# Kernel tuning notes

Hardware: AMD Instinct MI355X
Metric: run time of the kernel (lower is better)

Reference implementation:

```python
import jax, jax.numpy as jnp
import numpy as np

B, Lq, Lk = 2, 4096, 1024
Q_DIM, KV_DIM = 2048, 2048
H, HD = 16, 128          # n_heads, head_dim (nope part)
KVC, QC, R = 512, 768, 64  # kv_comp_dim, q_comp_dim, retr_dim (RoPE part)
LOOKBACK = 8
NEG = -1e30


def setup_inputs() -> dict:
    key = jax.random.key(0)
    ks = jax.random.split(key, 11)
    def w(k, shape, fan_in):
        return jax.random.normal(k, shape, jnp.float32) / np.sqrt(fan_in).astype(np.float32)
    return {
        'q': jax.random.normal(ks[0], (B, Lq, Q_DIM), jnp.float32),
        'kv': jax.random.normal(ks[1], (B, Lk, KV_DIM), jnp.float32),
        'seg_id': jnp.sort(jax.random.randint(ks[2], (B, Lq), 0, Lk), axis=-1),
        'W_kvc': w(ks[3], (KV_DIM, KVC), KV_DIM),   # kv_comp linear (no bias)
        'W_dq':  w(ks[4], (Q_DIM, QC), Q_DIM),      # query down-projection
        'W_uq':  w(ks[5], (QC, H * HD), QC),        # query up-proj (nope)
        'W_qr':  w(ks[6], (QC, H * R), QC),         # query rope proj
        'W_uk':  w(ks[7], (KVC, H * HD), KVC),      # key up-proj (nope)
        'W_kr':  w(ks[8], (KVC, R), KVC),           # shared key rope proj
        'W_uv':  w(ks[9], (KVC, H * HD), KVC),      # value up-proj
        'W_o':   w(ks[10], (H * HD, Q_DIM), H * HD),# output projection
    }


def _rope(x, L):
    # x: [..., L, R] with R even; positions 0..L-1 on the -2 axis.
    half = x.shape[-1] // 2
    inv_freq = 1.0 / (10000.0 ** (jnp.arange(half, dtype=jnp.float32) / half))
    ang = jnp.arange(L, dtype=jnp.float32)[:, None] * inv_freq  # [L, half]
    cos, sin = jnp.cos(ang), jnp.sin(ang)
    x1, x2 = x[..., :half], x[..., half:]
    return jnp.concatenate([x1 * cos - x2 * sin, x1 * sin + x2 * cos], axis=-1)


def reference(q, kv, seg_id, W_kvc, W_dq, W_uq, W_qr, W_uk, W_kr, W_uv, W_o):
    b, lq, _ = q.shape
    lk = kv.shape[1]
    kv_c = kv @ W_kvc                                   # [B,Lk,KVC]
    q_c = q @ W_dq                                      # [B,Lq,QC]
    q_nope = (q_c @ W_uq).reshape(b, lq, H, HD).transpose(0, 2, 1, 3)  # [B,H,Lq,HD]
    q_rope = (q_c @ W_qr).reshape(b, lq, H, R).transpose(0, 2, 1, 3)   # [B,H,Lq,R]
    k_nope = (kv_c @ W_uk).reshape(b, lk, H, HD)        # [B,Lk,H,HD]
    v = (kv_c @ W_uv).reshape(b, lk, H, HD)             # [B,Lk,H,HD]
    k_rope = kv_c @ W_kr                                # [B,Lk,R] shared across heads
    q_rope = _rope(q_rope, lq)
    k_rope = _rope(k_rope, lk)
    scale = 1.0 / np.sqrt(HD + R).astype(np.float32)
    scores = (jnp.einsum('bhqd,bkhd->bhqk', q_nope, k_nope)
              + jnp.einsum('bhqr,bkr->bhqk', q_rope, k_rope)) * scale
    # segment lookback block mask: allow q_seg - lookback <= k <= q_seg
    k_ids = jnp.arange(lk)[None, None, :]               # [1,1,Lk]
    qs = seg_id[:, :, None]                             # [B,Lq,1]
    good = (k_ids <= qs) & (k_ids >= qs - LOOKBACK)     # [B,Lq,Lk]
    scores = jnp.where(good[:, None, :, :], scores, NEG)
    attn = jax.nn.softmax(scores, axis=-1)              # [B,H,Lq,Lk]
    out = jnp.einsum('bhqk,bkhd->bqhd', attn, v).reshape(b, lq, H * HD)
    return out @ W_o                                    # [B,Lq,Q_DIM]
```

## Files before the change

### kernel.cpp

```cpp
#include <hip/hip_runtime.h>
#include <math.h>

typedef __bf16 bf16_t;
typedef __bf16 bf16x8 __attribute__((ext_vector_type(8)));
typedef float f32x4 __attribute__((ext_vector_type(4)));

#define B_    2
#define LQ    4096
#define LK    1024
#define QDIM  2048
#define KVDIM 2048
#define H_    16
#define HD_   128
#define KVC_  512
#define QC_   768
#define R_    64

#define QCOMB 3072
#define KCOMB 4352

#define NL_ROPE (-9.210340371976184f / 32.0f)

typedef __attribute__((address_space(1))) void gvoid_t;
typedef __attribute__((address_space(3))) void lvoid_t;

static __device__ __forceinline__ void gld_lds16(const void* g, void* l) {
  __builtin_amdgcn_global_load_lds((gvoid_t*)(void*)g, (lvoid_t*)l, 16, 0, 0);
}

static __device__ __forceinline__ float fexp(float x) {
  return __builtin_amdgcn_exp2f(x * 1.4426950408889634f);
}
static __device__ __forceinline__ void fsincos(float ang, float* s, float* c) {
  float rev = ang * 0.15915494309189535f;
  rev -= floorf(rev);
  *s = __builtin_amdgcn_sinf(rev);
  *c = __builtin_amdgcn_cosf(rev);
}

struct TransAll {
  const float* src[8];
  bf16_t* dst[8];
  int K[8], N[8], gx[8];
  int off[9];
};

#define NCVT 4096
__global__ __launch_bounds__(256) void prep_all(
    const float* __restrict__ qa, bf16_t* __restrict__ oq, long nq,
    const float* __restrict__ kva, bf16_t* __restrict__ okv, long nkv,
    TransAll d) {
  __shared__ float t[32][33];
  const int bid = blockIdx.x;
  if (bid < NCVT) {
    const long stride = (long)NCVT * 256 * 8;
    for (long i = ((long)bid * 256 + threadIdx.x) * 8; i < nq; i += stride) {
      float4 x = *(const float4*)(qa + i);
      float4 y = *(const float4*)(qa + i + 4);
      bf16x8 v;
      v[0] = (bf16_t)x.x; v[1] = (bf16_t)x.y; v[2] = (bf16_t)x.z; v[3] = (bf16_t)x.w;
      v[4] = (bf16_t)y.x; v[5] = (bf16_t)y.y; v[6] = (bf16_t)y.z; v[7] = (bf16_t)y.w;
      *(bf16x8*)(oq + i) = v;
    }
    for (long i = ((long)bid * 256 + threadIdx.x) * 8; i < nkv; i += stride) {
      float4 x = *(const float4*)(kva + i);
      float4 y = *(const float4*)(kva + i + 4);
      bf16x8 v;
      v[0] = (bf16_t)x.x; v[1] = (bf16_t)x.y; v[2] = (bf16_t)x.z; v[3] = (bf16_t)x.w;
      v[4] = (bf16_t)y.x; v[5] = (bf16_t)y.y; v[6] = (bf16_t)y.z; v[7] = (bf16_t)y.w;
      *(bf16x8*)(okv + i) = v;
    }
    return;
  }
  const int tb = bid - NCVT;
  int i = 0;
#pragma unroll
  for (int j = 1; j < 8; ++j) if (tb >= d.off[j]) i = j;
  const float* __restrict__ src = d.src[i];
  bf16_t* __restrict__ dst = d.dst[i];
  const int K = d.K[i], N = d.N[i];
  const int local = tb - d.off[i];
  const int gx = d.gx[i];
  const int bx = (local % gx) * 32, by = (local / gx) * 32;
  const int x = threadIdx.x & 31, y = threadIdx.x >> 5;
#pragma unroll
  for (int j = 0; j < 32; j += 8)
    t[y + j][x] = src[(size_t)(by + y + j) * N + bx + x];
  __syncthreads();
#pragma unroll
  for (int j = 0; j < 32; j += 8)
    dst[(size_t)(bx + y + j) * K + by + x] = (bf16_t)t[x][y + j];
}

template <int TN, typename CT>
__device__ __forceinline__ void big2_body(
    const bf16_t* __restrict__ A, const bf16_t* __restrict__ Bt, CT* __restrict__ C,
    int N, int K, int row0, int col0, bf16_t* lA, bf16_t* lB) {
  constexpr int NF = TN / 64;
  constexpr int LW = 4 + TN / 64;
  const int tid = threadIdx.x;
  const int w = tid >> 6, lane = tid & 63;
  const int wm = w >> 2, wn = w & 3;
  const int lr = lane >> 3;
  const int kswz = ((lane & 7) ^ lr) * 8;
  const int nt = K >> 6;
  const int fr = lane & 15, fq = lane >> 4;

  auto STAGE = [&](int t, int buf) {
    const int k0 = t << 6;
#pragma unroll
    for (int j = 0; j < 4; ++j) {
      const int s = j * 8 + w;
      gld_lds16(A + (size_t)(row0 + s * 8 + lr) * K + k0 + kswz, &lA[buf * 256 * 64 + s * 512]);
    }
#pragma unroll
    for (int j = 0; j < TN / 64; ++j) {
      const int s = j * 8 + w;
      gld_lds16(Bt + (size_t)(col0 + s * 8 + lr) * K + k0 + kswz, &lB[buf * TN * 64 + s * 512]);
    }
  };

  bf16x8 aA[8], bA[NF], aB[8], bB[NF];
  f32x4 acc[8][NF];
#pragma unroll
  for (int i = 0; i < 8; ++i)
#pragma unroll
    for (int j = 0; j < NF; ++j) acc[i][j] = f32x4{0.f, 0.f, 0.f, 0.f};

  auto READ = [&](int buf, int kk, bf16x8* a, bf16x8* b) {
    const int swzk = (kk * 32 + fq * 8) ^ ((fr & 7) << 3);
#pragma unroll
    for (int mf = 0; mf < 8; ++mf)
      a[mf] = *(const bf16x8*)&lA[buf * 256 * 64 + (wm * 128 + mf * 16 + fr) * 64 + swzk];
#pragma unroll
    for (int nf = 0; nf < NF; ++nf)
      b[nf] = *(const bf16x8*)&lB[buf * TN * 64 + (wn * (TN / 4) + nf * 16 + fr) * 64 + swzk];
  };
  auto MF = [&](bf16x8* a, bf16x8* b) {
    __builtin_amdgcn_s_setprio(1);
#pragma unroll
    for (int mf = 0; mf < 8; ++mf)
#pragma unroll
      for (int nf = 0; nf < NF; ++nf)
        acc[mf][nf] = __builtin_amdgcn_mfma_f32_16x16x32_bf16(a[mf], b[nf], acc[mf][nf], 0, 0, 0);
    __builtin_amdgcn_s_setprio(0);
  };

  STAGE(0, 0);
  STAGE(1, 1);
  if constexpr (LW == 8) { asm volatile("s_waitcnt vmcnt(8)" ::: "memory"); }
  else                   { asm volatile("s_waitcnt vmcnt(6)" ::: "memory"); }
  __builtin_amdgcn_sched_barrier(0);
  __builtin_amdgcn_s_barrier();
  READ(0, 0, aA, bA);

  for (int t = 0; t < nt; ++t) {
    const int buf = t & 1;
    READ(buf, 1, aB, bB);
    __builtin_amdgcn_sched_barrier(0);
    MF(aA, bA);
    asm volatile("s_waitcnt lgkmcnt(0)" ::: "memory");
    __builtin_amdgcn_sched_barrier(0);
    __builtin_amdgcn_s_barrier();
    if (t + 2 < nt) {
      STAGE(t + 2, buf);
      if constexpr (LW == 8) { asm volatile("s_waitcnt vmcnt(8)" ::: "memory"); }
      else                   { asm volatile("s_waitcnt vmcnt(6)" ::: "memory"); }
    } else {
      asm volatile("s_waitcnt vmcnt(0)" ::: "memory");
    }
    __builtin_amdgcn_sched_barrier(0);
    __builtin_amdgcn_s_barrier();
    if (t + 1 < nt) READ(buf ^ 1, 0, aA, bA);
    __builtin_amdgcn_sched_barrier(0);
    MF(aB, bB);
  }

#pragma unroll
  for (int mf = 0; mf < 8; ++mf)
#pragma unroll
    for (int nf = 0; nf < NF; ++nf) {
      const int col = col0 + wn * (TN / 4) + nf * 16 + fr;
#pragma unroll
      for (int r = 0; r < 4; ++r) {
        const int row = row0 + wm * 128 + mf * 16 + fq * 4 + r;
        C[(size_t)row * N + col] = (CT)acc[mf][nf][r];
      }
    }
}

__global__ __launch_bounds__(512, 2) void gemm_dual(
    const bf16_t* __restrict__ A0, const bf16_t* __restrict__ B0, bf16_t* __restrict__ C0,
    int N0, int K0,
    const bf16_t* __restrict__ A1, const bf16_t* __restrict__ B1, bf16_t* __restrict__ C1,
    int N1, int K1, int split) {
  __shared__ __align__(16) bf16_t lA[2 * 256 * 64];
  __shared__ __align__(16) bf16_t lB[2 * 128 * 64];
  const int nwg = gridDim.x;
  const int orig = blockIdx.x;
  const int wg = (orig & 7) * (nwg >> 3) + (orig >> 3);
  if (wg < split) {
    const int gx = N0 / 128;
    big2_body<128, bf16_t>(A0, B0, C0, N0, K0, (wg / gx) * 256, (wg % gx) * 128, lA, lB);
  } else {
    const int l = wg - split;
    const int gx = N1 / 128;
    big2_body<128, bf16_t>(A1, B1, C1, N1, K1, (l / gx) * 256, (l % gx) * 128, lA, lB);
  }
}

#define SWZK_(ks) (((ks) * 32 + fq * 8) ^ ((fr & 7) << 3))
#define RD_A(buf, q) { _Pragma("unroll") for (int mf = 0; mf < 4; ++mf) { \
    ar[mf][0] = *(const bf16x8*)&sA[((buf) * 2 + wm) * 8192 + ((q) * 64 + mf * 16 + fr) * 64 + SWZK_(0)]; \
    ar[mf][1] = *(const bf16x8*)&sA[((buf) * 2 + wm) * 8192 + ((q) * 64 + mf * 16 + fr) * 64 + SWZK_(1)]; } }
#define RD_B(buf, nq) { _Pragma("unroll") for (int nf = 0; nf < 2; ++nf) { \
    br[nq][nf][0] = *(const bf16x8*)&sB[((buf) * 2 + wbh) * 8192 + (wbr + (nq) * 32 + nf * 16 + fr) * 64 + SWZK_(0)]; \
    br[nq][nf][1] = *(const bf16x8*)&sB[((buf) * 2 + wbh) * 8192 + (wbr + (nq) * 32 + nf * 16 + fr) * 64 + SWZK_(1)]; } }
#define MFMA_Q(mq, nq) { __builtin_amdgcn_s_setprio(1); \
  _Pragma("unroll") for (int mf = 0; mf < 4; ++mf) \
  _Pragma("unroll") for (int nf = 0; nf < 2; ++nf) { \
    acc[(mq)*4+mf][(nq)*2+nf] = __builtin_amdgcn_mfma_f32_16x16x32_bf16(ar[mf][0], br[nq][nf][0], acc[(mq)*4+mf][(nq)*2+nf], 0, 0, 0); \
    acc[(mq)*4+mf][(nq)*2+nf] = __builtin_amdgcn_mfma_f32_16x16x32_bf16(ar[mf][1], br[nq][nf][1], acc[(mq)*4+mf][(nq)*2+nf], 0, 0, 0); } \
  __builtin_amdgcn_s_setprio(0); }
#define SBAR_ __builtin_amdgcn_sched_barrier(0)
#define HBAR_ __builtin_amdgcn_s_barrier()

template <typename CT>
__device__ __forceinline__ void ph8_body(
    const bf16_t* __restrict__ A, const bf16_t* __restrict__ Bt, CT* __restrict__ C,
    int N, int K, int row0, int col0, int ropeCol0, int posMask, bf16_t* sA, bf16_t* sB) {
  const int tid = threadIdx.x;
  const int w = tid >> 6, lane = tid & 63;
  const int wm = w >> 2, wn = w & 3;
  const int lr = lane >> 3;
  const int kswz = ((lane & 7) ^ lr) * 8;
  const int nt = K >> 6;
  const int fr = lane & 15, fq = lane >> 4;
  const int wbh = wn >> 1;
  const int wbr = (wn & 1) * 64;

  auto stA = [&](int t, int h, int buf) {
    const bf16_t* g = A + (size_t)(row0 + h * 128 + w * 8 + lr) * K + (t << 6) + kswz;
    gld_lds16(g, sA + (buf * 2 + h) * 8192 + w * 512);
    gld_lds16(g + (size_t)64 * K, sA + (buf * 2 + h) * 8192 + 4096 + w * 512);
  };
  auto stB = [&](int t, int h, int buf) {
    const bf16_t* g = Bt + (size_t)(col0 + h * 128 + w * 8 + lr) * K + (t << 6) + kswz;
    gld_lds16(g, sB + (buf * 2 + h) * 8192 + w * 512);
    gld_lds16(g + (size_t)64 * K, sB + (buf * 2 + h) * 8192 + 4096 + w * 512);
  };

  bf16x8 ar[4][2], br[2][2][2];
  f32x4 acc[8][4];
#pragma unroll
  for (int i = 0; i < 8; ++i)
#pragma unroll
    for (int j = 0; j < 4; ++j) acc[i][j] = f32x4{0.f, 0.f, 0.f, 0.f};

  stA(0, 0, 0); stA(0, 1, 0); stB(0, 0, 0); stB(0, 1, 0);
  stB(1, 0, 1); stB(1, 1, 1);
  asm volatile("s_waitcnt vmcnt(4)" ::: "memory");
  SBAR_; HBAR_;

  for (int t = 0; t < nt; ++t) {
    const int buf = t & 1;
    SBAR_;
    RD_A(buf, 0); RD_B(buf, 0);
    if (t + 1 < nt) stA(t + 1, 0, buf ^ 1);
    SBAR_; HBAR_;
    MFMA_Q(0, 0);
    SBAR_; HBAR_;
    SBAR_;
    RD_B(buf, 1);
    if (t + 1 < nt) stA(t + 1, 1, buf ^ 1);
    SBAR_; HBAR_;
    MFMA_Q(0, 1);
    SBAR_; HBAR_;
    SBAR_;
    RD_A(buf, 1);
    if (t + 2 < nt) stB(t + 2, 0, buf);
    SBAR_; HBAR_;
    MFMA_Q(1, 1);
    SBAR_; HBAR_;
    SBAR_;
    if (t + 2 < nt) {
      stB(t + 2, 1, buf);
      asm volatile("s_waitcnt vmcnt(4)" ::: "memory");
    } else {
      asm volatile("s_waitcnt vmcnt(0)" ::: "memory");
    }
    SBAR_; HBAR_; SBAR_;
    MFMA_Q(1, 0);
    SBAR_; HBAR_;
  }

  if (col0 >= ropeCol0) {
    const float if0 = fexp((float)fr * NL_ROPE);
    const float if1 = fexp((float)(fr + 16) * NL_ROPE);
    const size_t cbase = (size_t)col0 + wn * 64 + fr;
#pragma unroll
    for (int mfg = 0; mfg < 8; ++mfg)
#pragma unroll
      for (int r = 0; r < 4; ++r) {
        const int row = row0 + wm * 128 + mfg * 16 + fq * 4 + r;
        const float pos = (float)(row & posMask);
        float s0, c0, s1, c1;
        fsincos(pos * if0, &s0, &c0);
        fsincos(pos * if1, &s1, &c1);
        const float lo0 = acc[mfg][0][r], hi0 = acc[mfg][2][r];
        const float lo1 = acc[mfg][1][r], hi1 = acc[mfg][3][r];
        CT* cr = C + (size_t)row * N + cbase;
        cr[0]  = (CT)(lo0 * c0 - hi0 * s0);
        cr[16] = (CT)(lo1 * c1 - hi1 * s1);
        cr[32] = (CT)(lo0 * s0 + hi0 * c0);
        cr[48] = (CT)(lo1 * s1 + hi1 * c1);
      }
    return;
  }
#pragma unroll
  for (int mfg = 0; mfg < 8; ++mfg)
#pragma unroll
    for (int nfg = 0; nfg < 4; ++nfg) {
      const int col = col0 + wn * 64 + (nfg >> 1) * 32 + (nfg & 1) * 16 + fr;
#pragma unroll
      for (int r = 0; r < 4; ++r) {
        const int row = row0 + wm * 128 + mfg * 16 + fq * 4 + r;
        C[(size_t)row * N + col] = (CT)acc[mfg][nfg][r];
      }
    }
}

template <typename CT>
__global__ __launch_bounds__(512, 2) void gemm_8ph(
    const bf16_t* __restrict__ A, const bf16_t* __restrict__ Bt,
    CT* __restrict__ C, int M, int N, int K) {
  __shared__ __align__(16) bf16_t sA[2 * 2 * 128 * 64];
  __shared__ __align__(16) bf16_t sB[2 * 2 * 128 * 64];
  const int gx = gridDim.x;
  const int nwg = gx * gridDim.y;
  const int orig = blockIdx.y * gx + blockIdx.x;
  const int wg = (orig & 7) * (nwg >> 3) + (orig >> 3);
  const int bx = wg % gx, by = wg / gx;
  ph8_body<CT>(A, Bt, C, N, K, by * 256, bx * 256, 1 << 30, 0, sA, sB);
}

__global__ __launch_bounds__(512, 2) void gemm_up_fused(
    const bf16_t* __restrict__ A0, const bf16_t* __restrict__ B0, bf16_t* __restrict__ C0,
    int N0, int K0, int gx0,
    const bf16_t* __restrict__ A1, const bf16_t* __restrict__ B1, bf16_t* __restrict__ C1,
    int N1, int K1, int gx1, int split) {
  __shared__ __align__(16) bf16_t sA[2 * 2 * 128 * 64];
  __shared__ __align__(16) bf16_t sB[2 * 2 * 128 * 64];
  const int orig = blockIdx.x;
  if (orig < split) {
    const int wg = (orig & 7) * (split >> 3) + (orig >> 3);
    ph8_body<bf16_t>(A0, B0, C0, N0, K0, (wg / gx0) * 256, (wg % gx0) * 256, 2048, LQ - 1, sA, sB);
  } else {
    const int l = orig - split;
    const int n1 = gridDim.x - split;
    const int wg = (l & 7) * (n1 >> 3) + (l >> 3);
    ph8_body<bf16_t>(A1, B1, C1, N1, K1, (wg / gx1) * 256, (wg % gx1) * 256, 4096, LK - 1, sA, sB);
  }
}

__global__ __launch_bounds__(256) void attn_sparse(
    const bf16_t* __restrict__ qc, const bf16_t* __restrict__ kvc,
    const int* __restrict__ seg, bf16_t* __restrict__ out) {
  const int qrow = blockIdx.x * 4 + (threadIdx.x >> 6);
  const int lane = threadIdx.x & 63;
  const int h = lane >> 2, sub = lane & 3;
  const int b = qrow >> 12;
  const int s = seg[qrow];
  const int kl = max(0, s - 8);
  const float scale = 0.07216878364870322f;

  float qnf[32], qrf[16];
  {
    const bf16_t* p = qc + (size_t)qrow * QCOMB + h * HD_ + sub * 32;
#pragma unroll
    for (int j = 0; j < 4; ++j) {
      bf16x8 t = *(const bf16x8*)(p + j * 8);
#pragma unroll
      for (int e = 0; e < 8; ++e) qnf[j * 8 + e] = (float)t[e];
    }
    const bf16_t* p2 = qc + (size_t)qrow * QCOMB + 2048 + h * R_ + sub * 16;
#pragma unroll
    for (int j = 0; j < 2; ++j) {
      bf16x8 t = *(const bf16x8*)(p2 + j * 8);
#pragma unroll
      for (int e = 0; e < 8; ++e) qrf[j * 8 + e] = (float)t[e];
    }
  }

  float sc[9];
#pragma unroll
  for (int kk = 0; kk < 9; ++kk) {
    const int kx = kl + kk;
    const bf16_t* kb = kvc + (size_t)(b * LK + kx) * KCOMB;
    float d = 0.f;
    const bf16_t* p = kb + h * HD_ + sub * 32;
#pragma unroll
    for (int j = 0; j < 4; ++j) {
      bf16x8 t = *(const bf16x8*)(p + j * 8);
#pragma unroll
      for (int e = 0; e < 8; ++e) d += qnf[j * 8 + e] * (float)t[e];
    }
    const bf16_t* p2 = kb + 4096 + sub * 16;
#pragma unroll
    for (int j = 0; j < 2; ++j) {
      bf16x8 t = *(const bf16x8*)(p2 + j * 8);
#pragma unroll
      for (int e = 0; e < 8; ++e) d += qrf[j * 8 + e] * (float)t[e];
    }
    d += __shfl_xor(d, 1);
    d += __shfl_xor(d, 2);
    sc[kk] = (kx <= s) ? d * scale : -1e30f;
  }
  float m = sc[0];
#pragma unroll
  for (int kk = 1; kk < 9; ++kk) m = fmaxf(m, sc[kk]);
  float sum = 0.f;
#pragma unroll
  for (int kk = 0; kk < 9; ++kk) { const float p = expf(sc[kk] - m); sc[kk] = p; sum += p; }
  const float inv = 1.f / sum;

  float o[32];
#pragma unroll
  for (int j = 0; j < 32; ++j) o[j] = 0.f;
#pragma unroll
  for (int kk = 0; kk < 9; ++kk) {
    const bf16_t* pv = kvc + (size_t)(b * LK + kl + kk) * KCOMB + 2048 + h * HD_ + sub * 32;
    const float p = sc[kk] * inv;
#pragma unroll
    for (int j = 0; j < 4; ++j) {
      bf16x8 t = *(const bf16x8*)(pv + j * 8);
#pragma unroll
      for (int e = 0; e < 8; ++e) o[j * 8 + e] += p * (float)t[e];
    }
  }
  bf16_t* po = out + (size_t)qrow * (H_ * HD_) + h * HD_ + sub * 32;
#pragma unroll
  for (int j = 0; j < 4; ++j) {
    bf16x8 t;
#pragma unroll
    for (int e = 0; e < 8; ++e) t[e] = (bf16_t)o[j * 8 + e];
    *(bf16x8*)(po + j * 8) = t;
  }
}

extern "C" void kernel_launch(void* const* d_in, const int* in_sizes, int n_in,
                              void* d_out, int out_size, void* d_ws, size_t ws_size,
                              hipStream_t stream) {
  const float* q     = (const float*)d_in[0];
  const float* kv    = (const float*)d_in[1];
  const int*   seg   = (const int*)d_in[2];
  const float* W_kvc = (const float*)d_in[3];
  const float* W_dq  = (const float*)d_in[4];
  const float* W_uq  = (const float*)d_in[5];
  const float* W_qr  = (const float*)d_in[6];
  const float* W_uk  = (const float*)d_in[7];
  const float* W_kr  = (const float*)d_in[8];
  const float* W_uv  = (const float*)d_in[9];
  const float* W_o   = (const float*)d_in[10];
  float* out = (float*)d_out;
  (void)in_sizes; (void)n_in; (void)out_size; (void)ws_size;

  char* ws = (char*)d_ws;
  size_t off = 0;
  auto alloc = [&](size_t bytes) {
    char* p = ws + off;
    off = (off + bytes + 255) & ~(size_t)255;
    return p;
  };
  bf16_t* q_bf    = (bf16_t*)alloc((size_t)B_ * LQ * QDIM * 2);
  bf16_t* kv_bf   = (bf16_t*)alloc((size_t)B_ * LK * KVDIM * 2);
  bf16_t* WkvcT   = (bf16_t*)alloc((size_t)KVC_ * KVDIM * 2);
  bf16_t* WdqT    = (bf16_t*)alloc((size_t)QC_ * QDIM * 2);
  bf16_t* WuqrT   = (bf16_t*)alloc((size_t)QCOMB * QC_ * 2);
  bf16_t* WkvT    = (bf16_t*)alloc((size_t)KCOMB * KVC_ * 2);
  bf16_t* WoT     = (bf16_t*)alloc((size_t)QDIM * (H_ * HD_) * 2);
  bf16_t* kv_c    = (bf16_t*)alloc((size_t)B_ * LK * KVC_ * 2);
  bf16_t* q_c     = (bf16_t*)alloc((size_t)B_ * LQ * QC_ * 2);
  bf16_t* q_comb  = (bf16_t*)alloc((size_t)B_ * LQ * QCOMB * 2);
  bf16_t* kv_comb = (bf16_t*)alloc((size_t)B_ * LK * KCOMB * 2);
  bf16_t* attn_o  = q_bf;

  {
    TransAll d;
    auto set = [&](int i, const float* s, bf16_t* dt, int K, int N) {
      d.src[i] = s; d.dst[i] = dt; d.K[i] = K; d.N[i] = N; d.gx[i] = N / 32;
    };
    set(0, W_kvc, WkvcT, KVDIM, KVC_);
    set(1, W_dq,  WdqT,  QDIM,  QC_);
    set(2, W_uq,  WuqrT, QC_,   H_ * HD_);
    set(3, W_qr,  WuqrT + (size_t)(H_ * HD_) * QC_, QC_, H_ * R_);
    set(4, W_uk,  WkvT,  KVC_,  H_ * HD_);
    set(5, W_uv,  WkvT + (size_t)(H_ * HD_) * KVC_, KVC_, H_ * HD_);
    set(6, W_kr,  WkvT + (size_t)2 * (H_ * HD_) * KVC_, KVC_, R_);
    set(7, W_o,   WoT,   H_ * HD_, QDIM);
    int acc_off = 0;
    for (int i = 0; i < 8; ++i) {
      d.off[i] = acc_off;
      acc_off += (d.N[i] / 32) * (d.K[i] / 32);
    }
    d.off[8] = acc_off;
    prep_all<<<NCVT + acc_off, 256, 0, stream>>>(
        q, q_bf, (long)B_ * LQ * QDIM, kv, kv_bf, (long)B_ * LK * KVDIM, d);
  }

  gemm_dual<<<224, 512, 0, stream>>>(
      kv_bf, WkvcT, kv_c, KVC_, KVDIM,
      q_bf, WdqT, q_c, QC_, QDIM, 32);

  gemm_up_fused<<<520, 512, 0, stream>>>(
      q_c, WuqrT, q_comb, QCOMB, QC_, QCOMB / 256,
      kv_c, WkvT, kv_comb, KCOMB, KVC_, KCOMB / 256, 384);

  attn_sparse<<<(B_ * LQ) / 4, 256, 0, stream>>>(q_comb, kv_comb, seg, attn_o);

  gemm_8ph<float><<<dim3(QDIM / 256, (B_ * LQ) / 256), 512, 0, stream>>>(
      attn_o, WoT, out, B_ * LQ, QDIM, H_ * HD_);
}
```

Measured before the change: 275.2 us.

## Defer weight transposes into later kernels as extra blocks to overlap with compute

The single prep kernel that converted inputs and transposed all eight weights now transposes only the two down-projection weights. The up-projection weight transposes run as extra blocks appended to the down-projection GEMM launch, and the W_o transpose runs as extra blocks in the attention kernel. The goal is to take weight-transpose traffic off the critical path by overlapping it with GEMM and attention blocks that leave spare capacity. The cost is branchy kernels with extra LDS or scheduling pressure, and possible tail effects from the added blocks.

```diff
diff --git a/kernel.cpp b/kernel.cpp
--- a/kernel.cpp
+++ b/kernel.cpp
@@ -20,6 +20,8 @@
 #define KCOMB 4352
 
 #define NL_ROPE (-9.210340371976184f / 32.0f)
+#define NATT   ((B_ * LQ) / 4)
+#define WO_TILES 4096
 
 typedef __attribute__((address_space(1))) void gvoid_t;
 typedef __attribute__((address_space(3))) void lvoid_t;
@@ -45,12 +47,24 @@
   int off[9];
 };
 
+static __device__ __forceinline__ void trans_tile(
+    const float* __restrict__ src, bf16_t* __restrict__ dst, int K, int N,
+    int bx, int by, int x, int y, float* tb ) {
+#pragma unroll
+  for (int j = 0; j < 32; j += 8)
+    tb[(y + j) * 33 + x] = src[(size_t)(by + y + j) * N + bx + x];
+  __syncthreads();
+#pragma unroll
+  for (int j = 0; j < 32; j += 8)
+    dst[(size_t)(bx + y + j) * K + by + x] = (bf16_t)tb[x * 33 + (y + j)];
+}
+
 #define NCVT 4096
 __global__ __launch_bounds__(256) void prep_all(
     const float* __restrict__ qa, bf16_t* __restrict__ oq, long nq,
     const float* __restrict__ kva, bf16_t* __restrict__ okv, long nkv,
     TransAll d) {
-  __shared__ float t[32][33];
+  __shared__ float t[32 * 33];
   const int bid = blockIdx.x;
   if (bid < NCVT) {
     const long stride = (long)NCVT * 256 * 8;
@@ -76,20 +90,11 @@
   int i = 0;
 #pragma unroll
   for (int j = 1; j < 8; ++j) if (tb >= d.off[j]) i = j;
-  const float* __restrict__ src = d.src[i];
-  bf16_t* __restrict__ dst = d.dst[i];
-  const int K = d.K[i], N = d.N[i];
   const int local = tb - d.off[i];
   const int gx = d.gx[i];
-  const int bx = (local % gx) * 32, by = (local / gx) * 32;
-  const int x = threadIdx.x & 31, y = threadIdx.x >> 5;
-#pragma unroll
-  for (int j = 0; j < 32; j += 8)
-    t[y + j][x] = src[(size_t)(by + y + j) * N + bx + x];
-  __syncthreads();
-#pragma unroll
-  for (int j = 0; j < 32; j += 8)
-    dst[(size_t)(bx + y + j) * K + by + x] = (bf16_t)t[x][y + j];
+  trans_tile(d.src[i], d.dst[i], d.K[i], d.N[i],
+             (local % gx) * 32, (local / gx) * 32,
+             threadIdx.x & 31, threadIdx.x >> 5, t);
 }
 
 template <int TN, typename CT>
@@ -189,23 +194,35 @@
     }
 }
 
-__global__ __launch_bounds__(512, 2) void gemm_dual(
+__global__ __launch_bounds__(512, 2) void gemm_dual_prep(
     const bf16_t* __restrict__ A0, const bf16_t* __restrict__ B0, bf16_t* __restrict__ C0,
     int N0, int K0,
     const bf16_t* __restrict__ A1, const bf16_t* __restrict__ B1, bf16_t* __restrict__ C1,
-    int N1, int K1, int split) {
+    int N1, int K1, TransAll d) {
   __shared__ __align__(16) bf16_t lA[2 * 256 * 64];
   __shared__ __align__(16) bf16_t lB[2 * 128 * 64];
-  const int nwg = gridDim.x;
   const int orig = blockIdx.x;
-  const int wg = (orig & 7) * (nwg >> 3) + (orig >> 3);
-  if (wg < split) {
+  if (orig < 192) {
+    const int wg = (orig & 7) * 24 + (orig >> 3);
     const int gx = N0 / 128;
     big2_body<128, bf16_t>(A0, B0, C0, N0, K0, (wg / gx) * 256, (wg % gx) * 128, lA, lB);
+  } else if (orig < 224) {
+    const int l = orig - 192;
+    const int wg = (l & 7) * 4 + (l >> 3);
+    const int gx = N1 / 128;
+    big2_body<128, bf16_t>(A1, B1, C1, N1, K1, (wg / gx) * 256, (wg % gx) * 128, lA, lB);
   } else {
-    const int l = wg - split;
-    const int gx = N1 / 128;
-    big2_body<128, bf16_t>(A1, B1, C1, N1, K1, (l / gx) * 256, (l % gx) * 128, lA, lB);
+    const int grp = threadIdx.x >> 8;
+    const int tt = threadIdx.x & 255;
+    const int tile = (orig - 224) * 2 + grp;
+    int i = 0;
+#pragma unroll
+    for (int j = 1; j < 8; ++j) if (tile >= d.off[j]) i = j;
+    const int local = tile - d.off[i];
+    const int gx = d.gx[i];
+    float* tb = (float*)lA + grp * 32 * 33;
+    trans_tile(d.src[i], d.dst[i], d.K[i], d.N[i],
+               (local % gx) * 32, (local / gx) * 32, tt & 31, tt >> 5, tb);
   }
 }
 
@@ -365,7 +382,15 @@
 
 __global__ __launch_bounds__(256) void attn_sparse(
     const bf16_t* __restrict__ qc, const bf16_t* __restrict__ kvc,
-    const int* __restrict__ seg, bf16_t* __restrict__ out) {
+    const int* __restrict__ seg, bf16_t* __restrict__ out,
+    const float* __restrict__ Wo, bf16_t* __restrict__ WoT) {
+  __shared__ float tl[32 * 33];
+  if (blockIdx.x >= NATT) {
+    const int tile = blockIdx.x - NATT;
+    trans_tile(Wo, WoT, H_ * HD_, QDIM, (tile & 63) * 32, (tile >> 6) * 32,
+               threadIdx.x & 31, threadIdx.x >> 5, tl);
+    return;
+  }
   const int qrow = blockIdx.x * 4 + (threadIdx.x >> 6);
   const int lane = threadIdx.x & 63;
   const int h = lane >> 2, sub = lane & 3;
@@ -487,36 +512,42 @@
 
   {
     TransAll d;
-    auto set = [&](int i, const float* s, bf16_t* dt, int K, int N) {
+    d.src[0] = W_kvc; d.dst[0] = WkvcT; d.K[0] = KVDIM; d.N[0] = KVC_; d.gx[0] = KVC_ / 32;
+    d.src[1] = W_dq;  d.dst[1] = WdqT;  d.K[1] = QDIM;  d.N[1] = QC_;  d.gx[1] = QC_ / 32;
+    const int t0 = (KVC_ / 32) * (KVDIM / 32);
+    const int t1 = (QC_ / 32) * (QDIM / 32);
+    d.off[0] = 0; d.off[1] = t0;
+    for (int j = 2; j <= 8; ++j) d.off[j] = t0 + t1;
+    for (int j = 2; j < 8; ++j) { d.src[j] = W_kvc; d.dst[j] = WkvcT; d.K[j] = 32; d.N[j] = 32; d.gx[j] = 1; }
+    prep_all<<<NCVT + t0 + t1, 256, 0, stream>>>(
+        q, q_bf, (long)B_ * LQ * QDIM, kv, kv_bf, (long)B_ * LK * KVDIM, d);
+  }
+
+  {
+    TransAll d;
+    auto set = [&](int i, int prev_off, const float* s, bf16_t* dt, int K, int N) {
       d.src[i] = s; d.dst[i] = dt; d.K[i] = K; d.N[i] = N; d.gx[i] = N / 32;
+      d.off[i] = prev_off;
+      return prev_off + (N / 32) * (K / 32);
     };
-    set(0, W_kvc, WkvcT, KVDIM, KVC_);
-    set(1, W_dq,  WdqT,  QDIM,  QC_);
-    set(2, W_uq,  WuqrT, QC_,   H_ * HD_);
-    set(3, W_qr,  WuqrT + (size_t)(H_ * HD_) * QC_, QC_, H_ * R_);
-    set(4, W_uk,  WkvT,  KVC_,  H_ * HD_);
-    set(5, W_uv,  WkvT + (size_t)(H_ * HD_) * KVC_, KVC_, H_ * HD_);
-    set(6, W_kr,  WkvT + (size_t)2 * (H_ * HD_) * KVC_, KVC_, R_);
-    set(7, W_o,   WoT,   H_ * HD_, QDIM);
-    int acc_off = 0;
-    for (int i = 0; i < 8; ++i) {
-      d.off[i] = acc_off;
-      acc_off += (d.N[i] / 32) * (d.K[i] / 32);
-    }
-    d.off[8] = acc_off;
-    prep_all<<<NCVT + acc_off, 256, 0, stream>>>(
-        q, q_bf, (long)B_ * LQ * QDIM, kv, kv_bf, (long)B_ * LK * KVDIM, d);
-  }
-
-  gemm_dual<<<224, 512, 0, stream>>>(
-      kv_bf, WkvcT, kv_c, KVC_, KVDIM,
-      q_bf, WdqT, q_c, QC_, QDIM, 32);
+    int o2 = 0;
+    o2 = set(0, o2, W_uq, WuqrT, QC_, H_ * HD_);
+    o2 = set(1, o2, W_qr, WuqrT + (size_t)(H_ * HD_) * QC_, QC_, H_ * R_);
+    o2 = set(2, o2, W_uk, WkvT, KVC_, H_ * HD_);
+    o2 = set(3, o2, W_uv, WkvT + (size_t)(H_ * HD_) * KVC_, KVC_, H_ * HD_);
+    o2 = set(4, o2, W_kr, WkvT + (size_t)2 * (H_ * HD_) * KVC_, KVC_, R_);
+    for (int j = 5; j <= 8; ++j) d.off[j] = o2;
+    for (int j = 5; j < 8; ++j) { d.src[j] = W_uq; d.dst[j] = WuqrT; d.K[j] = 32; d.N[j] = 32; d.gx[j] = 1; }
+    gemm_dual_prep<<<224 + o2 / 2, 512, 0, stream>>>(
+        q_bf, WdqT, q_c, QC_, QDIM,
+        kv_bf, WkvcT, kv_c, KVC_, KVDIM, d);
+  }
 
   gemm_up_fused<<<520, 512, 0, stream>>>(
       q_c, WuqrT, q_comb, QCOMB, QC_, QCOMB / 256,
       kv_c, WkvT, kv_comb, KCOMB, KVC_, KCOMB / 256, 384);
 
-  attn_sparse<<<(B_ * LQ) / 4, 256, 0, stream>>>(q_comb, kv_comb, seg, attn_o);
+  attn_sparse<<<NATT + WO_TILES, 256, 0, stream>>>(q_comb, kv_comb, seg, attn_o, W_o, WoT);
 
   gemm_8ph<float><<<dim3(QDIM / 256, (B_ * LQ) / 256), 512, 0, stream>>>(
       attn_o, WoT, out, B_ * LQ, QDIM, H_ * HD_);
```

After: 285.4 us. 1.04x slower.
